# Kernel optimization log

Hardware: AMD Instinct MI355X
Metric: run time of the kernel (lower is better)

## Reference

```python
import jax, jax.numpy as jnp
import numpy as np

NUM_SPINS = 32
BATCH = 8192
HIDDEN = 1024
INPUT_DIM = 2
NUM_LAYERS = 1
EPS = 1e-12

# factorial table 0..NUM_SPINS in float32 (matches torch storing int factorials into float tensor)
_FACT = jnp.asarray(
    np.cumprod(np.concatenate([np.ones(1), np.arange(1, NUM_SPINS + 1, dtype=np.float64)])).astype(np.float32)
)


def setup_inputs() -> dict:
    key = jax.random.key(0)
    ks = jax.random.split(key, 7)
    bits = jax.random.randint(ks[0], (NUM_SPINS, BATCH), 0, 2)
    data_in = jax.nn.one_hot(bits, INPUT_DIM, dtype=jnp.float32)  # one-hot spin configs
    s = 1.0 / np.sqrt(HIDDEN)
    W_ih = jax.random.normal(ks[1], (HIDDEN, INPUT_DIM), jnp.float32) * s
    W_hh = jax.random.normal(ks[2], (HIDDEN, HIDDEN), jnp.float32) * s
    b_ih = jax.random.normal(ks[3], (HIDDEN,), jnp.float32) * s
    b_hh = jax.random.normal(ks[4], (HIDDEN,), jnp.float32) * s
    W_lin = jax.random.normal(ks[5], (INPUT_DIM, HIDDEN), jnp.float32) * s
    b_lin = jax.random.normal(ks[6], (INPUT_DIM,), jnp.float32) * s
    return {"data_in": data_in, "W_ih": W_ih, "W_hh": W_hh, "b_ih": b_ih,
            "b_hh": b_hh, "W_lin": W_lin, "b_lin": b_lin}


def _perm_w(n_idx, k):
    # n! / max(0,k)! * heaviside(k, 1)  -> 0 if k < 0, else fact ratio (1 at k==0 handled by ratio)
    k_i = jnp.clip(k, 0, NUM_SPINS).astype(jnp.int32)
    return _FACT[n_idx] / _FACT[k_i] * (k >= 0).astype(jnp.float32)


def _forward(data_in, W_ih, W_hh, b_ih, b_hh, W_lin, b_lin):
    N = NUM_SPINS
    B = data_in.shape[1]
    # shift inputs right by one spin; first input is init_state [1, 0]
    init = jnp.tile(jnp.array([1.0, 0.0], jnp.float32), (B, 1))
    data = jnp.concatenate([init[None], data_in[:-1]], axis=0)  # [N, B, 2]
    half = N // 2

    def step(carry, xs):
        h, cu, cd = carry
        x, s = xs  # x: [B, 2], s: spin index scalar
        for _ in range(NUM_LAYERS):  # same cell applied num_layers times, as in torch code
            h = jnp.tanh(x @ W_ih.T + b_ih + h @ W_hh.T + b_hh)
        p = jax.nn.softmax(h @ W_lin.T + b_lin, axis=1)  # [B, 2]
        mask = (s != 0).astype(jnp.float32)  # cum counts only updated for spin_num != 0
        cu = cu + mask * x[:, 0]
        cd = cd + mask * x[:, 1]
        up_w = _perm_w(N - s, half - cu) + EPS
        dn_w = _perm_w(N - s, half - cd) + EPS
        w = jnp.stack([up_w, dn_w], axis=1)  # [B, 2]
        p = jnp.where(s == 0, p, p * w)  # no weighting at first spin
        return (h, cu, cd), p

    h0 = jnp.zeros((B, HIDDEN), jnp.float32)
    z = jnp.zeros((B,), jnp.float32)
    _, probs = jax.lax.scan(step, (h0, z, z), (data, jnp.arange(N)))
    return probs / jnp.sum(probs, axis=2, keepdims=True)


def reference(data_in, W_ih, W_hh, b_ih, b_hh, W_lin, b_lin):
    return _forward(data_in, W_ih, W_hh, b_ih, b_hh, W_lin, b_lin)
```

## Files before the change

### kernel.cpp

```cpp
#include <hip/hip_runtime.h>


typedef __bf16 bf16;
typedef __bf16 bf16x8 __attribute__((ext_vector_type(8)));
typedef float  f32x4  __attribute__((ext_vector_type(4)));

#define HID   1024
#define BATCH 8192
#define NSPIN 32

#define AS1 __attribute__((address_space(1)))
#define AS3 __attribute__((address_space(3)))

__device__ __forceinline__ float tanh_fast(float x) {
    float ax = fabsf(x);
    float t  = __expf(-2.0f * ax);
    float r  = (1.0f - t) * __builtin_amdgcn_rcpf(1.0f + t);
    return __builtin_copysignf(r, x);
}


__global__ void prep1(const float* __restrict__ din, const float* __restrict__ Wih,
                      const float* __restrict__ Whh, const float* __restrict__ bih,
                      const float* __restrict__ bhh,
                      bf16* __restrict__ Wbf, float* __restrict__ u0, float* __restrict__ u1,
                      unsigned int* __restrict__ words, float* __restrict__ fact) {
    long idx = (long)blockIdx.x * blockDim.x + threadIdx.x;
    long stride = (long)gridDim.x * blockDim.x;
    for (long i = idx; i < (long)HID * HID; i += stride) Wbf[i] = (bf16)Whh[i];
    for (long i = idx; i < HID; i += stride) {
        u0[i] = Wih[i * 2 + 0] + bih[i] + bhh[i];
        u1[i] = Wih[i * 2 + 1] + bih[i] + bhh[i];
    }
    for (long b = idx; b < BATCH; b += stride) {
        unsigned int wv = 0;
        for (int j = 0; j < 31; ++j)
            wv |= (din[((long)j * BATCH + b) * 2 + 1] != 0.0f ? 1u : 0u) << j;
        words[b] = wv;
    }
    if (idx == 0) {
        double f = 1.0; fact[0] = 1.0f;
        for (int k = 1; k <= NSPIN; ++k) { f *= k; fact[k] = (float)f; }
    }
}

__global__ void prep2(const float* __restrict__ u0, const float* __restrict__ Wlin,
                      const float* __restrict__ blin,
                      bf16* __restrict__ hrow, float* __restrict__ l0s) {
    __shared__ float red0[16], red1[16];
    int t = threadIdx.x;
    float hv = tanh_fast(u0[t]);
    hrow[t] = (bf16)hv;
    float s0 = hv * Wlin[t], s1 = hv * Wlin[HID + t];
    #pragma unroll
    for (int off = 1; off < 64; off <<= 1) {
        s0 += __shfl_xor(s0, off, 64);
        s1 += __shfl_xor(s1, off, 64);
    }
    if ((t & 63) == 0) { red0[t >> 6] = s0; red1[t >> 6] = s1; }
    __syncthreads();
    if (t == 0) {
        float a = blin[0], b = blin[1];
        for (int i = 0; i < 16; ++i) { a += red0[i]; b += red1[i]; }
        l0s[0] = a; l0s[1] = b;
    }
}


__global__ __launch_bounds__(512, 2) void tree_step(
        const bf16* __restrict__ hin, bf16* __restrict__ hout,
        const bf16* __restrict__ Wbf,
        const float* __restrict__ u0, const float* __restrict__ u1,
        const float* __restrict__ Wlin,
        float* __restrict__ slog_s, int M) {
    __shared__ __align__(16) bf16 sA0[64 * 64];
    __shared__ __align__(16) bf16 sA1[64 * 64];
    __shared__ __align__(16) bf16 sA2[64 * 64];
    __shared__ __align__(16) bf16 sB0[128 * 64];
    __shared__ __align__(16) bf16 sB1[128 * 64];
    __shared__ __align__(16) bf16 sB2[128 * 64];

    const int tid = threadIdx.x;
    const int w = tid >> 6, l = tid & 63;
    const long rowM = (long)blockIdx.x * 64;
    const int  colN = blockIdx.y * 128;

    const int wr = w >> 2, wc = w & 3;
    const int fr = l & 15, fq = l >> 4;

    f32x4 acc[2][2] = {};

    const int lrow = l >> 3;
    const int lchk = l & 7;

#define TSTG(SA, SB, KT) do {                                                                \
    {   const int r_ = w * 8 + lrow;                                                         \
        const int sc_ = (lchk ^ (r_ & 7)) * 8;                                               \
        __builtin_amdgcn_global_load_lds(                                                    \
            (const AS1 void*)(hin + (rowM + r_) * HID + (KT) * 64 + sc_),                    \
            (AS3 void*)(&SA[(w * 8) * 64]), 16, 0, 0); }                                     \
    _Pragma("unroll")                                                                        \
    for (int i = 0; i < 2; ++i) {                                                            \
        const int r_ = w * 16 + i * 8 + lrow;                                                \
        const int sc_ = (lchk ^ (r_ & 7)) * 8;                                               \
        __builtin_amdgcn_global_load_lds(                                                    \
            (const AS1 void*)(Wbf + (long)(colN + r_) * HID + (KT) * 64 + sc_),              \
            (AS3 void*)(&SB[(w * 16 + i * 8) * 64]), 16, 0, 0);                              \
    }                                                                                        \
} while (0)

#define TBODY(CA, CB, NA, NB, T) do {                                                        \
    bf16x8 af[2][2], bf_[2][2];                                                              \
    _Pragma("unroll")                                                                        \
    for (int kk = 0; kk < 2; ++kk) {                                                         \
        _Pragma("unroll")                                                                    \
        for (int m = 0; m < 2; ++m) {                                                        \
            const int ra_ = wr * 32 + m * 16 + fr;                                           \
            af[kk][m] = *(const bf16x8*)&CA[ra_ * 64 + ((kk * 32 + fq * 8) ^ ((ra_ & 7) << 3))]; \
        }                                                                                    \
        _Pragma("unroll")                                                                    \
        for (int n = 0; n < 2; ++n) {                                                        \
            const int rb_ = wc * 32 + n * 16 + fr;                                           \
            bf_[kk][n] = *(const bf16x8*)&CB[rb_ * 64 + ((kk * 32 + fq * 8) ^ ((rb_ & 7) << 3))]; \
        }                                                                                    \
    }                                                                                        \
    if ((T) <= 13) TSTG(NA, NB, (T) + 2);                                                    \
    __builtin_amdgcn_s_setprio(1);                                                           \
    _Pragma("unroll")                                                                        \
    for (int kk = 0; kk < 2; ++kk)                                                           \
        _Pragma("unroll")                                                                    \
        for (int m = 0; m < 2; ++m)                                                          \
            _Pragma("unroll")                                                                \
            for (int n = 0; n < 2; ++n)                                                      \
                acc[m][n] = __builtin_amdgcn_mfma_f32_16x16x32_bf16(af[kk][m], bf_[kk][n], acc[m][n], 0, 0, 0); \
    __builtin_amdgcn_s_setprio(0);                                                           \
    __builtin_amdgcn_sched_barrier(0);                                                       \
    if ((T) <= 13)       asm volatile("s_waitcnt vmcnt(3)" ::: "memory");                    \
    else if ((T) == 14)  asm volatile("s_waitcnt vmcnt(0)" ::: "memory");                    \
    if ((T) <= 14) __builtin_amdgcn_s_barrier();                                             \
    __builtin_amdgcn_sched_barrier(0);                                                       \
} while (0)

    TSTG(sA0, sB0, 0);
    TSTG(sA1, sB1, 1);
    __builtin_amdgcn_sched_barrier(0);
    asm volatile("s_waitcnt vmcnt(3)" ::: "memory");
    __builtin_amdgcn_s_barrier();
    __builtin_amdgcn_sched_barrier(0);

    TBODY(sA0, sB0, sA2, sB2, 0);   TBODY(sA1, sB1, sA0, sB0, 1);
    TBODY(sA2, sB2, sA1, sB1, 2);   TBODY(sA0, sB0, sA2, sB2, 3);
    TBODY(sA1, sB1, sA0, sB0, 4);   TBODY(sA2, sB2, sA1, sB1, 5);
    TBODY(sA0, sB0, sA2, sB2, 6);   TBODY(sA1, sB1, sA0, sB0, 7);
    TBODY(sA2, sB2, sA1, sB1, 8);   TBODY(sA0, sB0, sA2, sB2, 9);
    TBODY(sA1, sB1, sA0, sB0, 10);  TBODY(sA2, sB2, sA1, sB1, 11);
    TBODY(sA0, sB0, sA2, sB2, 12);  TBODY(sA1, sB1, sA0, sB0, 13);
    TBODY(sA2, sB2, sA1, sB1, 14);  TBODY(sA0, sB0, sA2, sB2, 15);

#undef TBODY
#undef TSTG

    float u0v[2], u1v[2], wl0[2], wl1[2];
    int colg[2];
    #pragma unroll
    for (int n = 0; n < 2; ++n) {
        int c = colN + wc * 32 + n * 16 + fr;
        colg[n] = c;
        u0v[n] = u0[c]; u1v[n] = u1[c];
        wl0[n] = Wlin[c]; wl1[n] = Wlin[HID + c];
    }
    const int slot = blockIdx.y * 4 + wc;

    #pragma unroll
    for (int m = 0; m < 2; ++m) {
        #pragma unroll
        for (int r = 0; r < 4; ++r) {
            long p = rowM + wr * 32 + m * 16 + fq * 4 + r;
            if (p < M) {
                float s00 = 0.f, s01 = 0.f, s10 = 0.f, s11 = 0.f;
                #pragma unroll
                for (int n = 0; n < 2; ++n) {
                    float z  = acc[m][n][r];
                    float h0 = tanh_fast(z + u0v[n]);
                    float h1 = tanh_fast(z + u1v[n]);
                    hout[(2 * p + 0) * HID + colg[n]] = (bf16)h0;
                    hout[(2 * p + 1) * HID + colg[n]] = (bf16)h1;
                    s00 += h0 * wl0[n]; s01 += h0 * wl1[n];
                    s10 += h1 * wl0[n]; s11 += h1 * wl1[n];
                }
                #pragma unroll
                for (int off = 1; off < 16; off <<= 1) {
                    s00 += __shfl_xor(s00, off, 16);
                    s01 += __shfl_xor(s01, off, 16);
                    s10 += __shfl_xor(s10, off, 16);
                    s11 += __shfl_xor(s11, off, 16);
                }
                if (fr == 0) {
                    *(float2*)&slog_s[(2 * p + 0) * 64 + slot * 2] = make_float2(s00, s01);
                    *(float2*)&slog_s[(2 * p + 1) * 64 + slot * 2] = make_float2(s10, s11);
                }
            }
        }
    }
}

__global__ void gatherh(const bf16* __restrict__ states, const unsigned int* __restrict__ words,
                        bf16* __restrict__ hbatch) {
    long v = (long)blockIdx.x * blockDim.x + threadIdx.x;
    const long total = (long)BATCH * 128;
    for (; v < total; v += (long)gridDim.x * blockDim.x) {
        int b = (int)(v >> 7), c = (int)(v & 127);
        unsigned int p = __brev(words[b] & 0x1FFFu) >> 19;
        ((bf16x8*)hbatch)[v] = ((const bf16x8*)states)[(long)p * 128 + c];
    }
}


__global__ __launch_bounds__(512, 2) void gemm_step(
        const bf16* __restrict__ hin, bf16* __restrict__ hout,
        const bf16* __restrict__ Wbf,
        const float* __restrict__ u0, const float* __restrict__ u1,
        const unsigned int* __restrict__ words, int sbit,
        const float* __restrict__ Wlin,
        float* __restrict__ plog_s) {
    __shared__ __align__(16) bf16 sA0[128 * 64];
    __shared__ __align__(16) bf16 sA1[128 * 64];
    __shared__ __align__(16) bf16 sA2[128 * 64];
    __shared__ __align__(16) bf16 sB0[256 * 64];
    __shared__ __align__(16) bf16 sB1[256 * 64];
    __shared__ __align__(16) bf16 sB2[256 * 64];

    const int tid = threadIdx.x;
    const int w = tid >> 6, l = tid & 63;
    const long rowM = (long)blockIdx.x * 128;
    const int  colN = blockIdx.y * 256;

    const int wr = w >> 2, wc = w & 3;
    const int fr = l & 15, fq = l >> 4;

    f32x4 acc[4][4] = {};

    const int lrow = l >> 3;
    const int lchk = l & 7;

#define STG_A(SA, KT) do {                                                                   \
    _Pragma("unroll")                                                                        \
    for (int i = 0; i < 2; ++i) {                                                            \
        const int r_ = w * 16 + i * 8 + lrow;                                                \
        const int sc_ = (lchk ^ (r_ & 7)) * 8;                                               \
        __builtin_amdgcn_global_load_lds(                                                    \
            (const AS1 void*)(hin + (rowM + r_) * HID + (KT) * 64 + sc_),                    \
            (AS3 void*)(&SA[(w * 16 + i * 8) * 64]), 16, 0, 0);                              \
    }                                                                                        \
} while (0)

#define STG_B2(SB, KT, I0) do {                                                              \
    _Pragma("unroll")                                                                        \
    for (int i = (I0); i < (I0) + 2; ++i) {                                                  \
        const int r_ = w * 32 + i * 8 + lrow;                                                \
        const int sc_ = (lchk ^ (r_ & 7)) * 8;                                               \
        __builtin_amdgcn_global_load_lds(                                                    \
            (const AS1 void*)(Wbf + (long)(colN + r_) * HID + (KT) * 64 + sc_),              \
            (AS3 void*)(&SB[(w * 32 + i * 8) * 64]), 16, 0, 0);                              \
    }                                                                                        \
} while (0)

#define RD_FRAGS(AF, BF, SA, SB, KK) do {                                                    \
    _Pragma("unroll")                                                                        \
    for (int m = 0; m < 4; ++m) {                                                            \
        const int ra_ = wr * 64 + m * 16 + fr;                                               \
        AF[m] = *(const bf16x8*)&SA[ra_ * 64 + (((KK) * 32 + fq * 8) ^ ((ra_ & 7) << 3))];   \
    }                                                                                        \
    _Pragma("unroll")                                                                        \
    for (int n = 0; n < 4; ++n) {                                                            \
        const int rb_ = wc * 64 + n * 16 + fr;                                               \
        BF[n] = *(const bf16x8*)&SB[rb_ * 64 + (((KK) * 32 + fq * 8) ^ ((rb_ & 7) << 3))];   \
    }                                                                                        \
} while (0)

#define MFMA16(AF, BF) do {                                                                  \
    __builtin_amdgcn_s_setprio(1);                                                           \
    _Pragma("unroll")                                                                        \
    for (int m = 0; m < 4; ++m)                                                              \
        _Pragma("unroll")                                                                    \
        for (int n = 0; n < 4; ++n)                                                          \
            acc[m][n] = __builtin_amdgcn_mfma_f32_16x16x32_bf16(AF[m], BF[n], acc[m][n], 0, 0, 0); \
    __builtin_amdgcn_s_setprio(0);                                                           \
} while (0)

#define BODY(CA, CB, NA, NB, T) do {                                                         \
    bf16x8 afx[4], bfx[4], afy[4], bfy[4];                                                   \
    RD_FRAGS(afx, bfx, CA, CB, 0);                                                           \
    if ((T) <= 13) { STG_A(NA, (T) + 2); STG_B2(NB, (T) + 2, 0); }                           \
    MFMA16(afx, bfx);                                                                        \
    RD_FRAGS(afy, bfy, CA, CB, 1);                                                           \
    if ((T) <= 13) { STG_B2(NB, (T) + 2, 2); }                                               \
    MFMA16(afy, bfy);                                                                        \
    __builtin_amdgcn_sched_barrier(0);                                                       \
    if ((T) <= 13)       asm volatile("s_waitcnt vmcnt(6)" ::: "memory");                    \
    else if ((T) == 14)  asm volatile("s_waitcnt vmcnt(0)" ::: "memory");                    \
    if ((T) <= 14) __builtin_amdgcn_s_barrier();                                             \
    __builtin_amdgcn_sched_barrier(0);                                                       \
} while (0)

    STG_A(sA0, 0); STG_B2(sB0, 0, 0); STG_B2(sB0, 0, 2);
    STG_A(sA1, 1); STG_B2(sB1, 1, 0); STG_B2(sB1, 1, 2);
    __builtin_amdgcn_sched_barrier(0);
    asm volatile("s_waitcnt vmcnt(6)" ::: "memory");
    __builtin_amdgcn_s_barrier();
    __builtin_amdgcn_sched_barrier(0);

    BODY(sA0, sB0, sA2, sB2, 0);
    BODY(sA1, sB1, sA0, sB0, 1);
    BODY(sA2, sB2, sA1, sB1, 2);
    BODY(sA0, sB0, sA2, sB2, 3);
    BODY(sA1, sB1, sA0, sB0, 4);
    BODY(sA2, sB2, sA1, sB1, 5);
    BODY(sA0, sB0, sA2, sB2, 6);
    BODY(sA1, sB1, sA0, sB0, 7);
    BODY(sA2, sB2, sA1, sB1, 8);
    BODY(sA0, sB0, sA2, sB2, 9);
    BODY(sA1, sB1, sA0, sB0, 10);
    BODY(sA2, sB2, sA1, sB1, 11);
    BODY(sA0, sB0, sA2, sB2, 12);
    BODY(sA1, sB1, sA0, sB0, 13);
    BODY(sA2, sB2, sA1, sB1, 14);
    BODY(sA0, sB0, sA2, sB2, 15);

#undef BODY
#undef MFMA16
#undef RD_FRAGS
#undef STG_A
#undef STG_B2

    float u0v[4], u1v[4], wl0[4], wl1[4];
    int colg[4];
    #pragma unroll
    for (int n = 0; n < 4; ++n) {
        int c = colN + wc * 64 + n * 16 + fr;
        colg[n] = c;
        u0v[n] = u0[c]; u1v[n] = u1[c];
        wl0[n] = Wlin[c]; wl1[n] = Wlin[HID + c];
    }
    const int slot = blockIdx.y * 4 + wc;

    #pragma unroll
    for (int m = 0; m < 4; ++m) {
        #pragma unroll
        for (int r = 0; r < 4; ++r) {
            long rowg = rowM + wr * 64 + m * 16 + fq * 4 + r;
            int bt = (words[rowg] >> sbit) & 1;
            float s0 = 0.f, s1 = 0.f;
            #pragma unroll
            for (int n = 0; n < 4; ++n) {
                float z  = acc[m][n][r] + (bt ? u1v[n] : u0v[n]);
                float hv = tanh_fast(z);
                hout[rowg * HID + colg[n]] = (bf16)hv;
                s0 += hv * wl0[n];
                s1 += hv * wl1[n];
            }
            #pragma unroll
            for (int off = 1; off < 16; off <<= 1) {
                s0 += __shfl_xor(s0, off, 16);
                s1 += __shfl_xor(s1, off, 16);
            }
            if (fr == 0)
                *(float2*)&plog_s[rowg * 32 + slot * 2] = make_float2(s0, s1);
        }
    }
}


__global__ void finalize(const float* __restrict__ plog, const float* __restrict__ slog,
                         const float* __restrict__ l0s,
                         const float* __restrict__ blin, const unsigned int* __restrict__ words,
                         const float* __restrict__ fact, float* __restrict__ out) {
    long idx = (long)blockIdx.x * blockDim.x + threadIdx.x;
    if (idx >= (long)NSPIN * BATCH) return;
    int s = (int)(idx / BATCH), b = (int)(idx % BATCH);
    const unsigned int wv = words[b];

    float l0, l1;
    if (s == 0) { l0 = l0s[0]; l1 = l0s[1]; }
    else if (s <= 13) {
        unsigned int p = __brev(wv & ((1u << s) - 1)) >> (32 - s);
        const float* ps = slog + ((long)((1u << s) - 2) + p) * 64;
        l0 = blin[0]; l1 = blin[1];
        #pragma unroll
        for (int k = 0; k < 32; ++k) {
            l0 += ps[k * 2 + 0];
            l1 += ps[k * 2 + 1];
        }
    } else {
        l0 = blin[0]; l1 = blin[1];
        const float* ps = plog + ((long)(s - 14) * BATCH + b) * 32;
        #pragma unroll
        for (int k = 0; k < 16; ++k) {
            l0 += ps[k * 2 + 0];
            l1 += ps[k * 2 + 1];
        }
    }
    float mx = fmaxf(l0, l1);
    float e0 = __expf(l0 - mx), e1 = __expf(l1 - mx);
    float p0 = e0 / (e0 + e1), p1 = e1 / (e0 + e1);
    if (s > 0) {
        const int cd = __popc(wv & ((1u << s) - 1));
        const float cdf = (float)cd, cuf = (float)(s - cd);
        const float ku = 16.f - cuf, kd = 16.f - cdf;
        const int n = NSPIN - s;
        const int kui = (int)fminf(fmaxf(ku, 0.f), 32.f);
        const int kdi = (int)fminf(fmaxf(kd, 0.f), 32.f);
        const float wu = fact[n] / fact[kui] * (ku >= 0.f ? 1.f : 0.f) + 1e-12f;
        const float wd = fact[n] / fact[kdi] * (kd >= 0.f ? 1.f : 0.f) + 1e-12f;
        p0 *= wu; p1 *= wd;
    }
    float inv = 1.f / (p0 + p1);
    out[idx * 2 + 0] = p0 * inv;
    out[idx * 2 + 1] = p1 * inv;
}


extern "C" void kernel_launch(void* const* d_in, const int* in_sizes, int n_in,
                              void* d_out, int out_size, void* d_ws, size_t ws_size,
                              hipStream_t stream) {
    const float* din  = (const float*)d_in[0];
    const float* Wih  = (const float*)d_in[1];
    const float* Whh  = (const float*)d_in[2];
    const float* bih  = (const float*)d_in[3];
    const float* bhh  = (const float*)d_in[4];
    const float* Wlin = (const float*)d_in[5];
    const float* blin = (const float*)d_in[6];
    float* out = (float*)d_out;

    char* ws = (char*)d_ws;
    size_t o = 0;
    auto alloc = [&](size_t b) { size_t r = o; o += (b + 255) & ~(size_t)255; return r; };
    bf16*  Wbf  = (bf16*)(ws + alloc((size_t)HID * HID * 2));
    float* u0   = (float*)(ws + alloc(HID * 4));
    float* u1   = (float*)(ws + alloc(HID * 4));
    bf16*  hrow = (bf16*)(ws + alloc((size_t)64 * HID * 2));
    float* l0s  = (float*)(ws + alloc(2 * 4));
    float* fact = (float*)(ws + alloc(33 * 4));
    unsigned int* words = (unsigned int*)(ws + alloc((size_t)BATCH * 4));
    bf16*  hA   = (bf16*)(ws + alloc((size_t)BATCH * HID * 2));
    bf16*  hB   = (bf16*)(ws + alloc((size_t)BATCH * HID * 2));
    float* slog = (float*)(ws + alloc(((size_t)(1 << 14) - 2) * 64 * 4));
    float* plog = (float*)(ws + alloc(18L * BATCH * 32 * 4));

    prep1<<<1024, 256, 0, stream>>>(din, Wih, Whh, bih, bhh, Wbf, u0, u1, words, fact);
    prep2<<<1, 1024, 0, stream>>>(u0, Wlin, blin, hrow, l0s);

    const bf16* tin = hrow;
    bf16* tout = hA;
    for (int i = 1; i <= 13; ++i) {
        int Min = 1 << (i - 1);
        dim3 g(Min < 64 ? 1 : Min / 64, 8);
        tree_step<<<g, 512, 0, stream>>>(
            tin, tout, Wbf, u0, u1, Wlin,
            slog + ((long)(1 << i) - 2) * 64, Min);
        tin = tout;
        tout = (tout == hA) ? hB : hA;
    }
    gatherh<<<2048, 256, 0, stream>>>(tin, words, tout);

    bf16* hin = tout;
    bf16* hout = (tout == hA) ? hB : hA;
    for (int s = 14; s <= 31; ++s) {
        gemm_step<<<dim3(64, 4), 512, 0, stream>>>(
            hin, hout, Wbf, u0, u1, words, s - 1, Wlin,
            plog + (size_t)(s - 14) * BATCH * 32);
        bf16* t = hin; hin = hout; hout = t;
    }
    finalize<<<(NSPIN * BATCH) / 256, 256, 0, stream>>>(plog, slog, l0s, blin, words, fact, out);
}
```

Measured before the change: 600.4 us.

## Fuse first ten tree levels into one persistent kernel with grid barriers

Replaces the ten small tree_step launches for levels 1-10 with a single persistent 64-block kernel that loops over levels, synchronising blocks through an atomic counter barrier. This removes per-launch overhead and idle gaps for the tiny early levels. It also remaps gemm_step blocks so row tiles are grouped per XCD for better L2 locality, and skips writing the hidden state on the final step where it is never read. The spin-wait barrier depends on all 64 blocks being co-resident.

```diff
diff --git a/kernel.cpp b/kernel.cpp
--- a/kernel.cpp
+++ b/kernel.cpp
@@ -24,7 +24,8 @@
                       const float* __restrict__ Whh, const float* __restrict__ bih,
                       const float* __restrict__ bhh,
                       bf16* __restrict__ Wbf, float* __restrict__ u0, float* __restrict__ u1,
-                      unsigned int* __restrict__ words, float* __restrict__ fact) {
+                      unsigned int* __restrict__ words, float* __restrict__ fact,
+                      unsigned int* __restrict__ cnt) {
     long idx = (long)blockIdx.x * blockDim.x + threadIdx.x;
     long stride = (long)gridDim.x * blockDim.x;
     for (long i = idx; i < (long)HID * HID; i += stride) Wbf[i] = (bf16)Whh[i];
@@ -38,6 +39,7 @@
             wv |= (din[((long)j * BATCH + b) * 2 + 1] != 0.0f ? 1u : 0u) << j;
         words[b] = wv;
     }
+    if (idx < 16) cnt[idx] = 0;
     if (idx == 0) {
         double f = 1.0; fact[0] = 1.0f;
         for (int k = 1; k <= NSPIN; ++k) { f *= k; fact[k] = (float)f; }
@@ -67,6 +69,165 @@
 }
 
 
+#define TSTG(HIN, SA, SB, KT) do {                                                           \
+    {                                                                                        \
+        const int r_ = w * 8 + lrow;                                                         \
+        const int sc_ = (lchk ^ (r_ & 7)) * 8;                                               \
+        __builtin_amdgcn_global_load_lds(                                                    \
+            (const AS1 void*)((HIN) + (rowM + r_) * HID + (KT) * 64 + sc_),                  \
+            (AS3 void*)(&SA[(w * 8) * 64]), 16, 0, 0);                                       \
+    }                                                                                        \
+    _Pragma("unroll")                                                                        \
+    for (int i = 0; i < 2; ++i) {                                                            \
+        const int r_ = w * 16 + i * 8 + lrow;                                                \
+        const int sc_ = (lchk ^ (r_ & 7)) * 8;                                               \
+        __builtin_amdgcn_global_load_lds(                                                    \
+            (const AS1 void*)(Wbf + (long)(colN + r_) * HID + (KT) * 64 + sc_),              \
+            (AS3 void*)(&SB[(w * 16 + i * 8) * 64]), 16, 0, 0);                              \
+    }                                                                                        \
+} while (0)
+
+#define TBODY(HIN, CA, CB, NA, NB, T) do {                                                   \
+    bf16x8 af[2][2], bf_[2][2];                                                              \
+    _Pragma("unroll")                                                                        \
+    for (int kk = 0; kk < 2; ++kk) {                                                         \
+        _Pragma("unroll")                                                                    \
+        for (int m = 0; m < 2; ++m) {                                                        \
+            const int ra_ = wr * 32 + m * 16 + fr;                                           \
+            af[kk][m] = *(const bf16x8*)&CA[ra_ * 64 + ((kk * 32 + fq * 8) ^ ((ra_ & 7) << 3))]; \
+        }                                                                                    \
+        _Pragma("unroll")                                                                    \
+        for (int n = 0; n < 2; ++n) {                                                        \
+            const int rb_ = wc * 32 + n * 16 + fr;                                           \
+            bf_[kk][n] = *(const bf16x8*)&CB[rb_ * 64 + ((kk * 32 + fq * 8) ^ ((rb_ & 7) << 3))]; \
+        }                                                                                    \
+    }                                                                                        \
+    if ((T) <= 13) TSTG(HIN, NA, NB, (T) + 2);                                               \
+    __builtin_amdgcn_s_setprio(1);                                                           \
+    _Pragma("unroll")                                                                        \
+    for (int kk = 0; kk < 2; ++kk)                                                           \
+        _Pragma("unroll")                                                                    \
+        for (int m = 0; m < 2; ++m)                                                          \
+            _Pragma("unroll")                                                                \
+            for (int n = 0; n < 2; ++n)                                                      \
+                acc[m][n] = __builtin_amdgcn_mfma_f32_16x16x32_bf16(af[kk][m], bf_[kk][n], acc[m][n], 0, 0, 0); \
+    __builtin_amdgcn_s_setprio(0);                                                           \
+    __builtin_amdgcn_sched_barrier(0);                                                       \
+    if ((T) <= 13)       asm volatile("s_waitcnt vmcnt(3)" ::: "memory");                    \
+    else if ((T) == 14)  asm volatile("s_waitcnt vmcnt(0)" ::: "memory");                    \
+    if ((T) <= 14) __builtin_amdgcn_s_barrier();                                             \
+    __builtin_amdgcn_sched_barrier(0);                                                       \
+} while (0)
+
+#define TREE_KLOOP(HIN)                                                                      \
+    TSTG(HIN, sA0, sB0, 0);                                                                  \
+    TSTG(HIN, sA1, sB1, 1);                                                                  \
+    __builtin_amdgcn_sched_barrier(0);                                                       \
+    asm volatile("s_waitcnt vmcnt(3)" ::: "memory");                                         \
+    __builtin_amdgcn_s_barrier();                                                            \
+    __builtin_amdgcn_sched_barrier(0);                                                       \
+    TBODY(HIN, sA0, sB0, sA2, sB2, 0);   TBODY(HIN, sA1, sB1, sA0, sB0, 1);                  \
+    TBODY(HIN, sA2, sB2, sA1, sB1, 2);   TBODY(HIN, sA0, sB0, sA2, sB2, 3);                  \
+    TBODY(HIN, sA1, sB1, sA0, sB0, 4);   TBODY(HIN, sA2, sB2, sA1, sB1, 5);                  \
+    TBODY(HIN, sA0, sB0, sA2, sB2, 6);   TBODY(HIN, sA1, sB1, sA0, sB0, 7);                  \
+    TBODY(HIN, sA2, sB2, sA1, sB1, 8);   TBODY(HIN, sA0, sB0, sA2, sB2, 9);                  \
+    TBODY(HIN, sA1, sB1, sA0, sB0, 10);  TBODY(HIN, sA2, sB2, sA1, sB1, 11);                 \
+    TBODY(HIN, sA0, sB0, sA2, sB2, 12);  TBODY(HIN, sA1, sB1, sA0, sB0, 13);                 \
+    TBODY(HIN, sA2, sB2, sA1, sB1, 14);  TBODY(HIN, sA0, sB0, sA2, sB2, 15);
+
+#define TREE_EPILOGUE(HOUT, SLOG, M)                                                         \
+    float u0v[2], u1v[2], wl0[2], wl1[2];                                                    \
+    int colg[2];                                                                             \
+    _Pragma("unroll")                                                                        \
+    for (int n = 0; n < 2; ++n) {                                                            \
+        int c = colN + wc * 32 + n * 16 + fr;                                                \
+        colg[n] = c;                                                                         \
+        u0v[n] = u0[c]; u1v[n] = u1[c];                                                      \
+        wl0[n] = Wlin[c]; wl1[n] = Wlin[HID + c];                                            \
+    }                                                                                        \
+    const int slot = colPanel * 4 + wc;                                                      \
+    _Pragma("unroll")                                                                        \
+    for (int m = 0; m < 2; ++m) {                                                            \
+        _Pragma("unroll")                                                                    \
+        for (int r = 0; r < 4; ++r) {                                                        \
+            long p = rowM + wr * 32 + m * 16 + fq * 4 + r;                                   \
+            if (p < (M)) {                                                                   \
+                float s00 = 0.f, s01 = 0.f, s10 = 0.f, s11 = 0.f;                            \
+                _Pragma("unroll")                                                            \
+                for (int n = 0; n < 2; ++n) {                                                \
+                    float z  = acc[m][n][r];                                                 \
+                    float h0 = tanh_fast(z + u0v[n]);                                        \
+                    float h1 = tanh_fast(z + u1v[n]);                                        \
+                    (HOUT)[(2 * p + 0) * HID + colg[n]] = (bf16)h0;                          \
+                    (HOUT)[(2 * p + 1) * HID + colg[n]] = (bf16)h1;                          \
+                    s00 += h0 * wl0[n]; s01 += h0 * wl1[n];                                  \
+                    s10 += h1 * wl0[n]; s11 += h1 * wl1[n];                                  \
+                }                                                                            \
+                _Pragma("unroll")                                                            \
+                for (int off = 1; off < 16; off <<= 1) {                                     \
+                    s00 += __shfl_xor(s00, off, 16);                                         \
+                    s01 += __shfl_xor(s01, off, 16);                                         \
+                    s10 += __shfl_xor(s10, off, 16);                                         \
+                    s11 += __shfl_xor(s11, off, 16);                                         \
+                }                                                                            \
+                if (fr == 0) {                                                               \
+                    *(float2*)&(SLOG)[(2 * p + 0) * 64 + slot * 2] = make_float2(s00, s01);  \
+                    *(float2*)&(SLOG)[(2 * p + 1) * 64 + slot * 2] = make_float2(s10, s11);  \
+                }                                                                            \
+            }                                                                                \
+        }                                                                                    \
+    }
+
+
+__global__ __launch_bounds__(512, 2) void fused_tree(
+        const bf16* __restrict__ hrow, bf16* __restrict__ hA, bf16* __restrict__ hB,
+        const bf16* __restrict__ Wbf,
+        const float* __restrict__ u0, const float* __restrict__ u1,
+        const float* __restrict__ Wlin,
+        float* __restrict__ slog, unsigned int* __restrict__ cnt) {
+    __shared__ __align__(16) bf16 sA0[64 * 64];
+    __shared__ __align__(16) bf16 sA1[64 * 64];
+    __shared__ __align__(16) bf16 sA2[64 * 64];
+    __shared__ __align__(16) bf16 sB0[128 * 64];
+    __shared__ __align__(16) bf16 sB1[128 * 64];
+    __shared__ __align__(16) bf16 sB2[128 * 64];
+
+    const int tid = threadIdx.x;
+    const int w = tid >> 6, l = tid & 63;
+    const int px = blockIdx.x >> 3;
+    const int colPanel = blockIdx.x & 7;
+    const long rowM = (long)px * 64;
+    const int  colN = colPanel * 128;
+    const int wr = w >> 2, wc = w & 3;
+    const int fr = l & 15, fq = l >> 4;
+    const int lrow = l >> 3, lchk = l & 7;
+
+    const bf16* curin = hrow;
+    bf16* curout = hA;
+
+    for (int lvl = 1; lvl <= 10; ++lvl) {
+        const int M = 1 << (lvl - 1);
+        if (px < ((M + 63) >> 6)) {
+            f32x4 acc[2][2] = {};
+            float* slog_s = slog + ((long)(1 << lvl) - 2) * 64;
+            TREE_KLOOP(curin)
+            TREE_EPILOGUE(curout, slog_s, M)
+        }
+        __syncthreads();
+        if (tid == 0) {
+            __threadfence();
+            atomicAdd(&cnt[lvl], 1u);
+            while (__hip_atomic_load(&cnt[lvl], __ATOMIC_ACQUIRE,
+                                     __HIP_MEMORY_SCOPE_AGENT) < 64u)
+                __builtin_amdgcn_s_sleep(2);
+        }
+        __syncthreads();
+        curin = curout;
+        curout = (curout == hA) ? hB : hA;
+    }
+}
+
+
 __global__ __launch_bounds__(512, 2) void tree_step(
         const bf16* __restrict__ hin, bf16* __restrict__ hout,
         const bf16* __restrict__ Wbf,
@@ -83,125 +244,15 @@
     const int tid = threadIdx.x;
     const int w = tid >> 6, l = tid & 63;
     const long rowM = (long)blockIdx.x * 64;
-    const int  colN = blockIdx.y * 128;
-
+    const int  colPanel = blockIdx.y;
+    const int  colN = colPanel * 128;
     const int wr = w >> 2, wc = w & 3;
     const int fr = l & 15, fq = l >> 4;
+    const int lrow = l >> 3, lchk = l & 7;
 
     f32x4 acc[2][2] = {};
-
-    const int lrow = l >> 3;
-    const int lchk = l & 7;
-
-#define TSTG(SA, SB, KT) do {                                                                \
-    {   const int r_ = w * 8 + lrow;                                                         \
-        const int sc_ = (lchk ^ (r_ & 7)) * 8;                                               \
-        __builtin_amdgcn_global_load_lds(                                                    \
-            (const AS1 void*)(hin + (rowM + r_) * HID + (KT) * 64 + sc_),                    \
-            (AS3 void*)(&SA[(w * 8) * 64]), 16, 0, 0); }                                     \
-    _Pragma("unroll")                                                                        \
-    for (int i = 0; i < 2; ++i) {                                                            \
-        const int r_ = w * 16 + i * 8 + lrow;                                                \
-        const int sc_ = (lchk ^ (r_ & 7)) * 8;                                               \
-        __builtin_amdgcn_global_load_lds(                                                    \
-            (const AS1 void*)(Wbf + (long)(colN + r_) * HID + (KT) * 64 + sc_),              \
-            (AS3 void*)(&SB[(w * 16 + i * 8) * 64]), 16, 0, 0);                              \
-    }                                                                                        \
-} while (0)
-
-#define TBODY(CA, CB, NA, NB, T) do {                                                        \
-    bf16x8 af[2][2], bf_[2][2];                                                              \
-    _Pragma("unroll")                                                                        \
-    for (int kk = 0; kk < 2; ++kk) {                                                         \
-        _Pragma("unroll")                                                                    \
-        for (int m = 0; m < 2; ++m) {                                                        \
-            const int ra_ = wr * 32 + m * 16 + fr;                                           \
-            af[kk][m] = *(const bf16x8*)&CA[ra_ * 64 + ((kk * 32 + fq * 8) ^ ((ra_ & 7) << 3))]; \
-        }                                                                                    \
-        _Pragma("unroll")                                                                    \
-        for (int n = 0; n < 2; ++n) {                                                        \
-            const int rb_ = wc * 32 + n * 16 + fr;                                           \
-            bf_[kk][n] = *(const bf16x8*)&CB[rb_ * 64 + ((kk * 32 + fq * 8) ^ ((rb_ & 7) << 3))]; \
-        }                                                                                    \
-    }                                                                                        \
-    if ((T) <= 13) TSTG(NA, NB, (T) + 2);                                                    \
-    __builtin_amdgcn_s_setprio(1);                                                           \
-    _Pragma("unroll")                                                                        \
-    for (int kk = 0; kk < 2; ++kk)                                                           \
-        _Pragma("unroll")                                                                    \
-        for (int m = 0; m < 2; ++m)                                                          \
-            _Pragma("unroll")                                                                \
-            for (int n = 0; n < 2; ++n)                                                      \
-                acc[m][n] = __builtin_amdgcn_mfma_f32_16x16x32_bf16(af[kk][m], bf_[kk][n], acc[m][n], 0, 0, 0); \
-    __builtin_amdgcn_s_setprio(0);                                                           \
-    __builtin_amdgcn_sched_barrier(0);                                                       \
-    if ((T) <= 13)       asm volatile("s_waitcnt vmcnt(3)" ::: "memory");                    \
-    else if ((T) == 14)  asm volatile("s_waitcnt vmcnt(0)" ::: "memory");                    \
-    if ((T) <= 14) __builtin_amdgcn_s_barrier();                                             \
-    __builtin_amdgcn_sched_barrier(0);                                                       \
-} while (0)
-
-    TSTG(sA0, sB0, 0);
-    TSTG(sA1, sB1, 1);
-    __builtin_amdgcn_sched_barrier(0);
-    asm volatile("s_waitcnt vmcnt(3)" ::: "memory");
-    __builtin_amdgcn_s_barrier();
-    __builtin_amdgcn_sched_barrier(0);
-
-    TBODY(sA0, sB0, sA2, sB2, 0);   TBODY(sA1, sB1, sA0, sB0, 1);
-    TBODY(sA2, sB2, sA1, sB1, 2);   TBODY(sA0, sB0, sA2, sB2, 3);
-    TBODY(sA1, sB1, sA0, sB0, 4);   TBODY(sA2, sB2, sA1, sB1, 5);
-    TBODY(sA0, sB0, sA2, sB2, 6);   TBODY(sA1, sB1, sA0, sB0, 7);
-    TBODY(sA2, sB2, sA1, sB1, 8);   TBODY(sA0, sB0, sA2, sB2, 9);
-    TBODY(sA1, sB1, sA0, sB0, 10);  TBODY(sA2, sB2, sA1, sB1, 11);
-    TBODY(sA0, sB0, sA2, sB2, 12);  TBODY(sA1, sB1, sA0, sB0, 13);
-    TBODY(sA2, sB2, sA1, sB1, 14);  TBODY(sA0, sB0, sA2, sB2, 15);
-
-#undef TBODY
-#undef TSTG
-
-    float u0v[2], u1v[2], wl0[2], wl1[2];
-    int colg[2];
-    #pragma unroll
-    for (int n = 0; n < 2; ++n) {
-        int c = colN + wc * 32 + n * 16 + fr;
-        colg[n] = c;
-        u0v[n] = u0[c]; u1v[n] = u1[c];
-        wl0[n] = Wlin[c]; wl1[n] = Wlin[HID + c];
-    }
-    const int slot = blockIdx.y * 4 + wc;
-
-    #pragma unroll
-    for (int m = 0; m < 2; ++m) {
-        #pragma unroll
-        for (int r = 0; r < 4; ++r) {
-            long p = rowM + wr * 32 + m * 16 + fq * 4 + r;
-            if (p < M) {
-                float s00 = 0.f, s01 = 0.f, s10 = 0.f, s11 = 0.f;
-                #pragma unroll
-                for (int n = 0; n < 2; ++n) {
-                    float z  = acc[m][n][r];
-                    float h0 = tanh_fast(z + u0v[n]);
-                    float h1 = tanh_fast(z + u1v[n]);
-                    hout[(2 * p + 0) * HID + colg[n]] = (bf16)h0;
-                    hout[(2 * p + 1) * HID + colg[n]] = (bf16)h1;
-                    s00 += h0 * wl0[n]; s01 += h0 * wl1[n];
-                    s10 += h1 * wl0[n]; s11 += h1 * wl1[n];
-                }
-                #pragma unroll
-                for (int off = 1; off < 16; off <<= 1) {
-                    s00 += __shfl_xor(s00, off, 16);
-                    s01 += __shfl_xor(s01, off, 16);
-                    s10 += __shfl_xor(s10, off, 16);
-                    s11 += __shfl_xor(s11, off, 16);
-                }
-                if (fr == 0) {
-                    *(float2*)&slog_s[(2 * p + 0) * 64 + slot * 2] = make_float2(s00, s01);
-                    *(float2*)&slog_s[(2 * p + 1) * 64 + slot * 2] = make_float2(s10, s11);
-                }
-            }
-        }
-    }
+    TREE_KLOOP(hin)
+    TREE_EPILOGUE(hout, slog_s, M)
 }
 
 __global__ void gatherh(const bf16* __restrict__ states, const unsigned int* __restrict__ words,
@@ -220,7 +271,7 @@
         const bf16* __restrict__ hin, bf16* __restrict__ hout,
         const bf16* __restrict__ Wbf,
         const float* __restrict__ u0, const float* __restrict__ u1,
-        const unsigned int* __restrict__ words, int sbit,
+        const unsigned int* __restrict__ words, int sbit, int writeH,
         const float* __restrict__ Wlin,
         float* __restrict__ plog_s) {
     __shared__ __align__(16) bf16 sA0[128 * 64];
@@ -232,8 +283,12 @@
 
     const int tid = threadIdx.x;
     const int w = tid >> 6, l = tid & 63;
-    const long rowM = (long)blockIdx.x * 128;
-    const int  colN = blockIdx.y * 256;
+
+    const int lin = blockIdx.y * 64 + blockIdx.x;
+    const int xcd = lin & 7, jj = lin >> 3;
+    const long rowM = (long)(xcd * 8 + (jj >> 2)) * 128;
+    const int  by   = jj & 3;
+    const int  colN = by * 256;
 
     const int wr = w >> 2, wc = w & 3;
     const int fr = l & 15, fq = l >> 4;
@@ -342,7 +397,7 @@
         u0v[n] = u0[c]; u1v[n] = u1[c];
         wl0[n] = Wlin[c]; wl1[n] = Wlin[HID + c];
     }
-    const int slot = blockIdx.y * 4 + wc;
+    const int slot = by * 4 + wc;
 
     #pragma unroll
     for (int m = 0; m < 4; ++m) {
@@ -355,7 +410,7 @@
             for (int n = 0; n < 4; ++n) {
                 float z  = acc[m][n][r] + (bt ? u1v[n] : u0v[n]);
                 float hv = tanh_fast(z);
-                hout[rowg * HID + colg[n]] = (bf16)hv;
+                if (writeH) hout[rowg * HID + colg[n]] = (bf16)hv;
                 s0 += hv * wl0[n];
                 s1 += hv * wl1[n];
             }
@@ -441,21 +496,23 @@
     bf16*  hrow = (bf16*)(ws + alloc((size_t)64 * HID * 2));
     float* l0s  = (float*)(ws + alloc(2 * 4));
     float* fact = (float*)(ws + alloc(33 * 4));
+    unsigned int* cnt = (unsigned int*)(ws + alloc(16 * 4));
     unsigned int* words = (unsigned int*)(ws + alloc((size_t)BATCH * 4));
     bf16*  hA   = (bf16*)(ws + alloc((size_t)BATCH * HID * 2));
     bf16*  hB   = (bf16*)(ws + alloc((size_t)BATCH * HID * 2));
     float* slog = (float*)(ws + alloc(((size_t)(1 << 14) - 2) * 64 * 4));
     float* plog = (float*)(ws + alloc(18L * BATCH * 32 * 4));
 
-    prep1<<<1024, 256, 0, stream>>>(din, Wih, Whh, bih, bhh, Wbf, u0, u1, words, fact);
+    prep1<<<1024, 256, 0, stream>>>(din, Wih, Whh, bih, bhh, Wbf, u0, u1, words, fact, cnt);
     prep2<<<1, 1024, 0, stream>>>(u0, Wlin, blin, hrow, l0s);
 
-    const bf16* tin = hrow;
+    fused_tree<<<64, 512, 0, stream>>>(hrow, hA, hB, Wbf, u0, u1, Wlin, slog, cnt);
+
+    const bf16* tin = hB;
     bf16* tout = hA;
-    for (int i = 1; i <= 13; ++i) {
+    for (int i = 11; i <= 13; ++i) {
         int Min = 1 << (i - 1);
-        dim3 g(Min < 64 ? 1 : Min / 64, 8);
-        tree_step<<<g, 512, 0, stream>>>(
+        tree_step<<<dim3(Min / 64, 8), 512, 0, stream>>>(
             tin, tout, Wbf, u0, u1, Wlin,
             slog + ((long)(1 << i) - 2) * 64, Min);
         tin = tout;
@@ -467,7 +524,7 @@
     bf16* hout = (tout == hA) ? hB : hA;
     for (int s = 14; s <= 31; ++s) {
         gemm_step<<<dim3(64, 4), 512, 0, stream>>>(
-            hin, hout, Wbf, u0, u1, words, s - 1, Wlin,
+            hin, hout, Wbf, u0, u1, words, s - 1, (s < 31) ? 1 : 0, Wlin,
             plog + (size_t)(s - 14) * BATCH * 32);
         bf16* t = hin; hin = hout; hout = t;
     }
```

Result: slower. 677.9 us (+12.9%).
